# Performance work log

Measured on AMD Instinct MI355X. Metric: run time of the kernel, lower is better.

Reference implementation:

```python
import jax, jax.numpy as jnp
import numpy as np

# pywt Wavelet('db4').rec_lo (scaling/reconstruction lowpass filter, 8 taps)
_REC_LO_DB4 = np.array([
    0.23037781330885523, 0.7148465705525415, 0.6308807679295904,
    -0.02798376941698385, -0.18703481171888114, 0.030841381835986965,
    0.032883011666982945, -0.010597401784997278], dtype=np.float64)
LEVEL = 3


def _filters(dtype):
    h = jnp.asarray(_REC_LO_DB4, dtype=dtype)          # rec_lo
    dec_lo = h[::-1]                                    # dec_lo = rec_lo reversed
    signs = jnp.asarray((-1.0) ** (np.arange(h.shape[0]) + 1), dtype=dtype)
    dec_hi = signs * h                                  # dec_hi = qmf(rec_lo) reversed
    return dec_lo, dec_hi


def _dwt_per(x, dec_lo, dec_hi):
    # periodization-mode single-level DWT: cA[i] = sum_j f[j] * x[(2i+1-j) mod N]
    N = x.shape[-1]
    L = dec_lo.shape[0]
    i = np.arange(N // 2)
    j = np.arange(L)
    idx = (2 * i[:, None] + 1 - j[None, :]) % N         # [N/2, L] static gather indices
    win = x[:, idx]                                     # [B, N/2, L]
    return win @ dec_lo, win @ dec_hi


def _idwt_per(cA, cD, dec_lo, dec_hi):
    # inverse = adjoint (orthogonal wavelet, periodization):
    # x[n] = sum_{j: (n+j-1) even mod N} dec_lo[j]*cA[((n+j-1)%N)//2] + dec_hi[j]*cD[...]
    M = cA.shape[-1]
    N = 2 * M
    L = dec_lo.shape[0]
    n = np.arange(N)
    j = np.arange(L)
    t = (n[:, None] + j[None, :] - 1) % N               # [N, L]
    even = jnp.asarray(t % 2 == 0)
    src = t // 2                                        # valid cA/cD index when even
    zero = jnp.zeros((), dtype=cA.dtype)
    coefA = jnp.where(even, dec_lo[None, :], zero)      # [N, L]
    coefD = jnp.where(even, dec_hi[None, :], zero)
    return (jnp.einsum('bnl,nl->bn', cA[:, src], coefA)
            + jnp.einsum('bnl,nl->bn', cD[:, src], coefD))


def setup_inputs() -> dict:
    key = jax.random.key(0)
    detrended = jax.random.normal(key, (2048, 4096), dtype=jnp.float32)
    return {"detrended": detrended}


def reference(detrended):
    B, S = detrended.shape
    dec_lo, dec_hi = _filters(detrended.dtype)
    blk = 2 ** LEVEL
    pad = (-S) % blk
    x = jnp.pad(detrended, ((0, 0), (0, pad)), mode='reflect') if pad else detrended
    # wavedec: [cA_L, cD_L, ..., cD_1]
    a = x
    details = []
    for _ in range(LEVEL):
        a, d = _dwt_per(a, dec_lo, dec_hi)
        details.append(d)
    # zero out coarsest approximation -> seasonal = waverec([0, cD_L, ..., cD_1])
    a = jnp.zeros_like(a)
    for d in reversed(details):
        a = _idwt_per(a, d, dec_lo, dec_hi)
    seasonal = a[:, :S]
    residual = detrended - seasonal
    return seasonal, residual
```

## Files before the change

kernel.cpp:

```cpp
#include <hip/hip_runtime.h>

static constexpr float LO[8] = {
    -0.010597401784997278f,  0.032883011666982945f,  0.030841381835986965f,
    -0.18703481171888114f,  -0.02798376941698385f,   0.6308807679295904f,
     0.7148465705525415f,    0.23037781330885523f
};
static constexpr float HI[8] = {
    -0.23037781330885523f,   0.7148465705525415f,   -0.6308807679295904f,
    -0.02798376941698385f,   0.18703481171888114f,   0.030841381835986965f,
    -0.032883011666982945f, -0.010597401784997278f
};

template<int N, bool WANT_A>
__device__ __forceinline__ void dwt_level(const float* __restrict__ x,
                                          float* __restrict__ a,
                                          float* __restrict__ d,
                                          int t)
{
    constexpr int M = N / 2;
    constexpr int ITERS = M / 512;
    #pragma unroll
    for (int k = 0; k < ITERS; ++k) {
        const int i0 = 2 * (t + 256 * k);
        float w[10];
        #pragma unroll
        for (int c = 0; c < 5; ++c) {
            const int idx = (2 * i0 - 6 + 2 * c + N) & (N - 1);
            const float2 v = *(const float2*)(x + idx);
            w[2 * c] = v.x; w[2 * c + 1] = v.y;
        }
        float a0 = 0.f, a1 = 0.f, d0 = 0.f, d1 = 0.f;
        #pragma unroll
        for (int kk = 0; kk < 8; ++kk) {
            if (WANT_A) {
                a0 = fmaf(w[kk],     LO[7 - kk], a0);
                a1 = fmaf(w[kk + 2], LO[7 - kk], a1);
            }
            d0 = fmaf(w[kk],     HI[7 - kk], d0);
            d1 = fmaf(w[kk + 2], HI[7 - kk], d1);
        }
        if (WANT_A) *(float2*)(a + i0) = make_float2(a0, a1);
        *(float2*)(d + i0) = make_float2(d0, d1);
    }
}

template<int M, bool HAS_A>
__device__ __forceinline__ void idwt_level(const float* __restrict__ cA,
                                           const float* __restrict__ cD,
                                           float* __restrict__ out,
                                           int t)
{
    constexpr int ITERS = M / 512;
    #pragma unroll
    for (int k = 0; k < ITERS; ++k) {
        const int m0 = 2 * (t + 256 * k);
        float av[6], dv[6];
        #pragma unroll
        for (int c = 0; c < 3; ++c) {
            const int idx = (m0 + 2 * c) & (M - 1);
            if (HAS_A) {
                const float2 v = *(const float2*)(cA + idx);
                av[2 * c] = v.x; av[2 * c + 1] = v.y;
            }
            const float2 v2 = *(const float2*)(cD + idx);
            dv[2 * c] = v2.x; dv[2 * c + 1] = v2.y;
        }
        float s0 = 0.f, s1 = 0.f, s2 = 0.f, s3 = 0.f;
        #pragma unroll
        for (int q = 0; q < 4; ++q) {
            if (HAS_A) {
                s0 = fmaf(av[q],     LO[2 * q + 1], s0);
                s1 = fmaf(av[q],     LO[2 * q],     s1);
                s2 = fmaf(av[q + 1], LO[2 * q + 1], s2);
                s3 = fmaf(av[q + 1], LO[2 * q],     s3);
            }
            s0 = fmaf(dv[q],     HI[2 * q + 1], s0);
            s1 = fmaf(dv[q],     HI[2 * q],     s1);
            s2 = fmaf(dv[q + 1], HI[2 * q + 1], s2);
            s3 = fmaf(dv[q + 1], HI[2 * q],     s3);
        }
        *(float4*)(out + 2 * m0) = make_float4(s0, s1, s2, s3);
    }
}

__global__ __launch_bounds__(256)
void WaveletSeasonalDecomposer_43181601194295_kernel(const float* __restrict__ in,
                                                     float* __restrict__ seasonal,
                                                     float* __restrict__ residual)
{
    __shared__ __align__(16) float arena[8192];
    const int t = threadIdx.x;
    const int row = blockIdx.x;

    const float4* in4 = (const float4*)(in + (size_t)row * 4096);
    float4 xr[4];
    #pragma unroll
    for (int k = 0; k < 4; ++k) {
        const float4 v = in4[t + 256 * k];
        xr[k] = v;
        ((float4*)arena)[t + 256 * k] = v;
    }
    __syncthreads();

    dwt_level<4096, true >(arena,        arena + 4096, arena + 6144, t);
    __syncthreads();
    dwt_level<2048, true >(arena + 4096, arena,        arena + 1024, t);
    __syncthreads();
    dwt_level<1024, false>(arena,        nullptr,      arena + 2048, t);
    __syncthreads();
    idwt_level<512,  false>(nullptr,       arena + 2048, arena + 2560, t);
    __syncthreads();
    idwt_level<1024, true >(arena + 2560,  arena + 1024, arena + 4096, t);
    __syncthreads();

    const float* X1 = arena + 4096;
    const float* D1 = arena + 6144;
    float4* outS4 = (float4*)(seasonal + (size_t)row * 4096);
    float4* outR4 = (float4*)(residual + (size_t)row * 4096);
    #pragma unroll
    for (int k = 0; k < 4; ++k) {
        const int m0 = 2 * (t + 256 * k);
        float av[6], dv[6];
        #pragma unroll
        for (int c = 0; c < 3; ++c) {
            const int idx = (m0 + 2 * c) & 2047;
            const float2 v  = *(const float2*)(X1 + idx);
            av[2 * c] = v.x;  av[2 * c + 1] = v.y;
            const float2 v2 = *(const float2*)(D1 + idx);
            dv[2 * c] = v2.x; dv[2 * c + 1] = v2.y;
        }
        float s0 = 0.f, s1 = 0.f, s2 = 0.f, s3 = 0.f;
        #pragma unroll
        for (int q = 0; q < 4; ++q) {
            s0 = fmaf(av[q],     LO[2 * q + 1], s0);
            s1 = fmaf(av[q],     LO[2 * q],     s1);
            s2 = fmaf(av[q + 1], LO[2 * q + 1], s2);
            s3 = fmaf(av[q + 1], LO[2 * q],     s3);
            s0 = fmaf(dv[q],     HI[2 * q + 1], s0);
            s1 = fmaf(dv[q],     HI[2 * q],     s1);
            s2 = fmaf(dv[q + 1], HI[2 * q + 1], s2);
            s3 = fmaf(dv[q + 1], HI[2 * q],     s3);
        }
        const float4 s = make_float4(s0, s1, s2, s3);
        const float4 x = xr[k];
        const float4 r = make_float4(x.x - s0, x.y - s1, x.z - s2, x.w - s3);
        outS4[t + 256 * k] = s;
        outR4[t + 256 * k] = r;
    }
}

extern "C" void kernel_launch(void* const* d_in, const int* in_sizes, int n_in,
                              void* d_out, int out_size, void* d_ws, size_t ws_size,
                              hipStream_t stream) {
    const float* in = (const float*)d_in[0];
    const int rows = in_sizes[0] / 4096;
    float* seasonal = (float*)d_out;
    float* residual = seasonal + (size_t)rows * 4096;
    WaveletSeasonalDecomposer_43181601194295_kernel<<<dim3(rows), dim3(256), 0, stream>>>(
        in, seasonal, residual);
}
```

Baseline: 91.90 us.

## Process one row per wavefront in registers with shuffle halo exchange

Replaces the block-per-row shared-memory pipeline with a wave-per-row scheme. Each lane holds 64 contiguous samples in registers and runs all three DWT and IDWT levels there, getting boundary halos from neighbouring lanes through __shfl instead of LDS with __syncthreads. This removes shared-memory traffic and block barriers. In exchange, each lane issues strided, uncoalesced 256-byte-per-lane global loads and stores, and register pressure rises a lot, with spill risk under launch_bounds(256,2).

```diff
diff --git a/kernel.cpp b/kernel.cpp
--- a/kernel.cpp
+++ b/kernel.cpp
@@ -11,141 +11,166 @@
     -0.032883011666982945f, -0.010597401784997278f
 };
 
-template<int N, bool WANT_A>
-__device__ __forceinline__ void dwt_level(const float* __restrict__ x,
-                                          float* __restrict__ a,
-                                          float* __restrict__ d,
-                                          int t)
-{
-    constexpr int M = N / 2;
-    constexpr int ITERS = M / 512;
-    #pragma unroll
-    for (int k = 0; k < ITERS; ++k) {
-        const int i0 = 2 * (t + 256 * k);
-        float w[10];
-        #pragma unroll
-        for (int c = 0; c < 5; ++c) {
-            const int idx = (2 * i0 - 6 + 2 * c + N) & (N - 1);
-            const float2 v = *(const float2*)(x + idx);
-            w[2 * c] = v.x; w[2 * c + 1] = v.y;
-        }
-        float a0 = 0.f, a1 = 0.f, d0 = 0.f, d1 = 0.f;
-        #pragma unroll
-        for (int kk = 0; kk < 8; ++kk) {
-            if (WANT_A) {
-                a0 = fmaf(w[kk],     LO[7 - kk], a0);
-                a1 = fmaf(w[kk + 2], LO[7 - kk], a1);
-            }
-            d0 = fmaf(w[kk],     HI[7 - kk], d0);
-            d1 = fmaf(w[kk + 2], HI[7 - kk], d1);
-        }
-        if (WANT_A) *(float2*)(a + i0) = make_float2(a0, a1);
-        *(float2*)(d + i0) = make_float2(d0, d1);
-    }
-}
-
-template<int M, bool HAS_A>
-__device__ __forceinline__ void idwt_level(const float* __restrict__ cA,
-                                           const float* __restrict__ cD,
-                                           float* __restrict__ out,
-                                           int t)
-{
-    constexpr int ITERS = M / 512;
-    #pragma unroll
-    for (int k = 0; k < ITERS; ++k) {
-        const int m0 = 2 * (t + 256 * k);
-        float av[6], dv[6];
-        #pragma unroll
-        for (int c = 0; c < 3; ++c) {
-            const int idx = (m0 + 2 * c) & (M - 1);
-            if (HAS_A) {
-                const float2 v = *(const float2*)(cA + idx);
-                av[2 * c] = v.x; av[2 * c + 1] = v.y;
-            }
-            const float2 v2 = *(const float2*)(cD + idx);
-            dv[2 * c] = v2.x; dv[2 * c + 1] = v2.y;
-        }
-        float s0 = 0.f, s1 = 0.f, s2 = 0.f, s3 = 0.f;
-        #pragma unroll
-        for (int q = 0; q < 4; ++q) {
-            if (HAS_A) {
-                s0 = fmaf(av[q],     LO[2 * q + 1], s0);
-                s1 = fmaf(av[q],     LO[2 * q],     s1);
-                s2 = fmaf(av[q + 1], LO[2 * q + 1], s2);
-                s3 = fmaf(av[q + 1], LO[2 * q],     s3);
-            }
-            s0 = fmaf(dv[q],     HI[2 * q + 1], s0);
-            s1 = fmaf(dv[q],     HI[2 * q],     s1);
-            s2 = fmaf(dv[q + 1], HI[2 * q + 1], s2);
-            s3 = fmaf(dv[q + 1], HI[2 * q],     s3);
-        }
-        *(float4*)(out + 2 * m0) = make_float4(s0, s1, s2, s3);
-    }
-}
-
-__global__ __launch_bounds__(256)
+__global__ __launch_bounds__(256, 2)
 void WaveletSeasonalDecomposer_43181601194295_kernel(const float* __restrict__ in,
                                                      float* __restrict__ seasonal,
                                                      float* __restrict__ residual)
 {
-    __shared__ __align__(16) float arena[8192];
-    const int t = threadIdx.x;
-    const int row = blockIdx.x;
+    const int lane = threadIdx.x & 63;
+    const int wave = threadIdx.x >> 6;
+    const int row  = (blockIdx.x << 2) + wave;
+    const int prev = (lane + 63) & 63;
+    const int next = (lane + 1) & 63;
 
-    const float4* in4 = (const float4*)(in + (size_t)row * 4096);
-    float4 xr[4];
+    const size_t rbase = (size_t)row * 4096 + (size_t)lane * 64;
+    const float* xr = in + rbase;
+
+    float x[64];
     #pragma unroll
-    for (int k = 0; k < 4; ++k) {
-        const float4 v = in4[t + 256 * k];
-        xr[k] = v;
-        ((float4*)arena)[t + 256 * k] = v;
+    for (int c = 0; c < 16; ++c) {
+        const float4 v = *(const float4*)(xr + 4 * c);
+        x[4 * c + 0] = v.x; x[4 * c + 1] = v.y;
+        x[4 * c + 2] = v.z; x[4 * c + 3] = v.w;
     }
-    __syncthreads();
 
-    dwt_level<4096, true >(arena,        arena + 4096, arena + 6144, t);
-    __syncthreads();
-    dwt_level<2048, true >(arena + 4096, arena,        arena + 1024, t);
-    __syncthreads();
-    dwt_level<1024, false>(arena,        nullptr,      arena + 2048, t);
-    __syncthreads();
-    idwt_level<512,  false>(nullptr,       arena + 2048, arena + 2560, t);
-    __syncthreads();
-    idwt_level<1024, true >(arena + 2560,  arena + 1024, arena + 4096, t);
-    __syncthreads();
+    float hx[6];
+    #pragma unroll
+    for (int k = 0; k < 6; ++k) hx[k] = __shfl(x[58 + k], prev, 64);
 
-    const float* X1 = arena + 4096;
-    const float* D1 = arena + 6144;
-    float4* outS4 = (float4*)(seasonal + (size_t)row * 4096);
-    float4* outR4 = (float4*)(residual + (size_t)row * 4096);
+    float a1[32], d1[32];
     #pragma unroll
-    for (int k = 0; k < 4; ++k) {
-        const int m0 = 2 * (t + 256 * k);
-        float av[6], dv[6];
+    for (int i = 0; i < 32; ++i) {
+        float sa = 0.f, sd = 0.f;
         #pragma unroll
-        for (int c = 0; c < 3; ++c) {
-            const int idx = (m0 + 2 * c) & 2047;
-            const float2 v  = *(const float2*)(X1 + idx);
-            av[2 * c] = v.x;  av[2 * c + 1] = v.y;
-            const float2 v2 = *(const float2*)(D1 + idx);
-            dv[2 * c] = v2.x; dv[2 * c + 1] = v2.y;
+        for (int j = 0; j < 8; ++j) {
+            const int idx = 2 * i + 1 - j;
+            const float v = (idx >= 0) ? x[idx >= 0 ? idx : 0]
+                                       : hx[idx < 0 ? idx + 6 : 0];
+            sa = fmaf(v, LO[j], sa);
+            sd = fmaf(v, HI[j], sd);
         }
-        float s0 = 0.f, s1 = 0.f, s2 = 0.f, s3 = 0.f;
+        a1[i] = sa; d1[i] = sd;
+    }
+
+    float h2[6];
+    #pragma unroll
+    for (int k = 0; k < 6; ++k) h2[k] = __shfl(a1[26 + k], prev, 64);
+
+    float a2[16], d2[16];
+    #pragma unroll
+    for (int i = 0; i < 16; ++i) {
+        float sa = 0.f, sd = 0.f;
+        #pragma unroll
+        for (int j = 0; j < 8; ++j) {
+            const int idx = 2 * i + 1 - j;
+            const float v = (idx >= 0) ? a1[idx >= 0 ? idx : 0]
+                                       : h2[idx < 0 ? idx + 6 : 0];
+            sa = fmaf(v, LO[j], sa);
+            sd = fmaf(v, HI[j], sd);
+        }
+        a2[i] = sa; d2[i] = sd;
+    }
+
+    float h3[6];
+    #pragma unroll
+    for (int k = 0; k < 6; ++k) h3[k] = __shfl(a2[10 + k], prev, 64);
+
+    float d3[8];
+    #pragma unroll
+    for (int i = 0; i < 8; ++i) {
+        float sd = 0.f;
+        #pragma unroll
+        for (int j = 0; j < 8; ++j) {
+            const int idx = 2 * i + 1 - j;
+            const float v = (idx >= 0) ? a2[idx >= 0 ? idx : 0]
+                                       : h3[idx < 0 ? idx + 6 : 0];
+            sd = fmaf(v, HI[j], sd);
+        }
+        d3[i] = sd;
+    }
+
+    float hd3[3];
+    #pragma unroll
+    for (int k = 0; k < 3; ++k) hd3[k] = __shfl(d3[k], next, 64);
+
+    float x2[16];
+    #pragma unroll
+    for (int m = 0; m < 8; ++m) {
+        float e0 = 0.f, e1 = 0.f;
         #pragma unroll
         for (int q = 0; q < 4; ++q) {
-            s0 = fmaf(av[q],     LO[2 * q + 1], s0);
-            s1 = fmaf(av[q],     LO[2 * q],     s1);
-            s2 = fmaf(av[q + 1], LO[2 * q + 1], s2);
-            s3 = fmaf(av[q + 1], LO[2 * q],     s3);
-            s0 = fmaf(dv[q],     HI[2 * q + 1], s0);
-            s1 = fmaf(dv[q],     HI[2 * q],     s1);
-            s2 = fmaf(dv[q + 1], HI[2 * q + 1], s2);
-            s3 = fmaf(dv[q + 1], HI[2 * q],     s3);
+            const int idx = m + q;
+            const float v = (idx < 8) ? d3[idx < 8 ? idx : 0]
+                                      : hd3[idx >= 8 ? idx - 8 : 0];
+            e0 = fmaf(v, HI[2 * q + 1], e0);
+            e1 = fmaf(v, HI[2 * q],     e1);
         }
-        const float4 s = make_float4(s0, s1, s2, s3);
-        const float4 x = xr[k];
-        const float4 r = make_float4(x.x - s0, x.y - s1, x.z - s2, x.w - s3);
-        outS4[t + 256 * k] = s;
-        outR4[t + 256 * k] = r;
+        x2[2 * m] = e0; x2[2 * m + 1] = e1;
+    }
+
+    float hA2i[3], hD2i[3];
+    #pragma unroll
+    for (int k = 0; k < 3; ++k) {
+        hA2i[k] = __shfl(x2[k], next, 64);
+        hD2i[k] = __shfl(d2[k], next, 64);
+    }
+
+    float x1[32];
+    #pragma unroll
+    for (int m = 0; m < 16; ++m) {
+        float e0 = 0.f, e1 = 0.f;
+        #pragma unroll
+        for (int q = 0; q < 4; ++q) {
+            const int idx = m + q;
+            const float va = (idx < 16) ? x2[idx < 16 ? idx : 0]
+                                        : hA2i[idx >= 16 ? idx - 16 : 0];
+            const float vd = (idx < 16) ? d2[idx < 16 ? idx : 0]
+                                        : hD2i[idx >= 16 ? idx - 16 : 0];
+            e0 = fmaf(va, LO[2 * q + 1], e0);
+            e1 = fmaf(va, LO[2 * q],     e1);
+            e0 = fmaf(vd, HI[2 * q + 1], e0);
+            e1 = fmaf(vd, HI[2 * q],     e1);
+        }
+        x1[2 * m] = e0; x1[2 * m + 1] = e1;
+    }
+
+    float hA1i[3], hD1i[3];
+    #pragma unroll
+    for (int k = 0; k < 3; ++k) {
+        hA1i[k] = __shfl(x1[k], next, 64);
+        hD1i[k] = __shfl(d1[k], next, 64);
+    }
+
+    float* sr = seasonal + rbase;
+    float* rr = residual + rbase;
+
+    #pragma unroll
+    for (int m = 0; m < 32; m += 2) {
+        float s[4];
+        #pragma unroll
+        for (int mm = 0; mm < 2; ++mm) {
+            float e0 = 0.f, e1 = 0.f;
+            #pragma unroll
+            for (int q = 0; q < 4; ++q) {
+                const int idx = m + mm + q;
+                const float va = (idx < 32) ? x1[idx < 32 ? idx : 0]
+                                            : hA1i[idx >= 32 ? idx - 32 : 0];
+                const float vd = (idx < 32) ? d1[idx < 32 ? idx : 0]
+                                            : hD1i[idx >= 32 ? idx - 32 : 0];
+                e0 = fmaf(va, LO[2 * q + 1], e0);
+                e1 = fmaf(va, LO[2 * q],     e1);
+                e0 = fmaf(vd, HI[2 * q + 1], e0);
+                e1 = fmaf(vd, HI[2 * q],     e1);
+            }
+            s[2 * mm]     = e0;
+            s[2 * mm + 1] = e1;
+        }
+        const int n0 = 2 * m;
+        const float4 sv = make_float4(s[0], s[1], s[2], s[3]);
+        const float4 rv = make_float4(x[n0 + 0] - s[0], x[n0 + 1] - s[1],
+                                      x[n0 + 2] - s[2], x[n0 + 3] - s[3]);
+        *(float4*)(sr + n0) = sv;
+        *(float4*)(rr + n0) = rv;
     }
 }
 
@@ -156,6 +181,6 @@
     const int rows = in_sizes[0] / 4096;
     float* seasonal = (float*)d_out;
     float* residual = seasonal + (size_t)rows * 4096;
-    WaveletSeasonalDecomposer_43181601194295_kernel<<<dim3(rows), dim3(256), 0, stream>>>(
+    WaveletSeasonalDecomposer_43181601194295_kernel<<<dim3(rows / 4), dim3(256), 0, stream>>>(
         in, seasonal, residual);
 }
```

Result: slower. 137.5 us (+49.6%).
